# Performance work log

Hardware: AMD Instinct MI355X
Metric: run time of the kernel (lower is better)

The kernel has to match this reference:

```python
import jax, jax.numpy as jnp
import numpy as np

DT = 0.01
SIGMA_RECUR = 0.005
SIGMA_INPUT = 0.05


def setup_inputs() -> dict:
    key = jax.random.key(0)
    ks = jax.random.split(key, 13)
    B, T, I, H = 64, 1000, 4, 512
    H2 = 2 * H
    return {
        "inp": jax.random.normal(ks[0], (B, T, I), jnp.float32),
        "hn": jax.random.uniform(ks[1], (1, B, H2), jnp.float32),
        "x": jax.random.normal(ks[2], (1, B, H2), jnp.float32),
        "inhib_stim": jax.random.normal(ks[3], (B, H2), jnp.float32),
        "perturb_hid": jax.random.normal(ks[4], (T,), jnp.float32),
        "perturb_inp": jax.random.normal(ks[5], (T,), jnp.float32),
        "str2str": jax.random.uniform(ks[6], (H, H), jnp.float32, -0.01, 0.01),
        "alm2alm": jax.random.uniform(ks[7], (H, H), jnp.float32, -0.01, 0.01),
        "alm2str": jax.random.uniform(ks[8], (H, H), jnp.float32, -0.01, 0.01),
        "str2alm": jax.random.uniform(ks[9], (H, H), jnp.float32, -0.01, 0.01),
        "inp_weight": jax.random.uniform(ks[10], (I, H2), jnp.float32, -0.01, 0.01),
        "fc1_w": jax.random.uniform(ks[11], (1, H2), jnp.float32, -0.03, 0.03),
        "fc1_b": jnp.zeros((1,), jnp.float32),
    }


def reference(inp, hn, x, inhib_stim, perturb_hid, perturb_inp,
              str2str, alm2alm, alm2str, str2alm, inp_weight, fc1_w, fc1_b):
    H = str2str.shape[0]
    # W_rec: [[str2str, alm2str], [str2alm, alm2alm]] -> (2H, 2H)
    W_rec = jnp.concatenate([
        jnp.concatenate([str2str, alm2str], axis=1),
        jnp.concatenate([str2alm, alm2alm], axis=1),
    ], axis=0)
    str_mask = jnp.concatenate([jnp.ones((H,), inp.dtype), jnp.zeros((H,), inp.dtype)])
    alm_mask = jnp.concatenate([jnp.zeros((H,), inp.dtype), jnp.ones((H,), inp.dtype)])

    # scalar per-step noise, as in the original (single Normal draw per t)
    ph = jnp.sqrt(2 * DT * SIGMA_RECUR ** 2) * perturb_hid  # [T]
    pi = jnp.sqrt(2 * DT * SIGMA_INPUT ** 2) * perturb_inp  # [T]

    h0 = hn[0]  # [B, 2H]
    x0 = x[0]   # [B, 2H]

    def step(carry, xs_t):
        h_prev, x_prev = carry
        inp_t, ph_t, pi_t = xs_t  # inp_t: [B, I]
        drive = (inp_t + pi_t) @ inp_weight  # [B, 2H]
        x_new = x_prev + DT * (-x_prev + h_prev @ W_rec.T
                               + drive * str_mask + inhib_stim) + ph_t
        h_new = jax.nn.relu(x_new)
        return (h_new, x_new), (h_new, x_new)

    inp_t_major = jnp.transpose(inp, (1, 0, 2))  # [T, B, I]
    (_, _), (hs, xs) = jax.lax.scan(step, (h0, x0), (inp_t_major, ph, pi))

    rnn_out = jnp.transpose(hs, (1, 0, 2))  # [B, T, 2H]
    x_out = jnp.transpose(xs, (1, 0, 2))    # [B, T, 2H]
    hn_last = rnn_out[:, -1, :][None]       # [1, B, 2H]
    x_last = x_out[:, -1, :][None]
    out = (rnn_out * alm_mask) @ fc1_w.T + fc1_b  # [B, T, 1]
    return (out, hn_last, rnn_out, x_last, x_out)
```

## Files before the change

kernel.cpp:

```cpp
#include <hip/hip_runtime.h>
#include <hip/hip_bf16.h>

#define TT 1000
#define HH 512
#define HH2 1024
#define DT_ 0.01f
#define PH_SCALE 7.0710678118654745e-4f
#define PI_SCALE 7.0710678118654745e-3f

typedef short s16x8 __attribute__((ext_vector_type(8)));
typedef float f32x4 __attribute__((ext_vector_type(4)));
typedef unsigned u32x4 __attribute__((ext_vector_type(4)));

#define SIGN32  0x80008000u
#define STRIP32 0x7fff7fffu

static __device__ __forceinline__ unsigned short bf16_bits(float f) {
    union { __hip_bfloat16 h; unsigned short u; } b; b.h = __float2bfloat16(f); return b.u;
}
static __device__ __forceinline__ unsigned pat32(int t) {
    const unsigned tg = ((unsigned)t >> 1) & 3u;
    return ((tg & 1u) << 15) | ((tg & 2u) << 30);
}

__global__ __launch_bounds__(256, 1) void rnn_persistent(
    const float* __restrict__ inp, const float* __restrict__ hn,
    const float* __restrict__ x0g, const float* __restrict__ inhib,
    const float* __restrict__ ph, const float* __restrict__ pig,
    const float* __restrict__ s2s, const float* __restrict__ a2a,
    const float* __restrict__ a2s, const float* __restrict__ s2a,
    const float* __restrict__ iw,
    float* __restrict__ rnn_out, float* __restrict__ x_out,
    unsigned* __restrict__ hbuf)
{
    const int tid  = threadIdx.x;
    const int wid  = tid >> 6;
    const int lane = tid & 63;
    const int b    = blockIdx.x;
    const int g    = b >> 4;
    const int qb   = b & 15;
    const int l15  = lane & 15;
    const int lq   = lane >> 4;
    const int r8   = l15 & 7;
    const int g8   = g * 8;
    const int icol = (qb * 4 + wid) * 16 + l15;
    const bool owner = (lq < 2);
    const int rowbase = g8 + (lq & 1) * 4;

    __shared__ __align__(16) unsigned short hlds[2][8 * 1024];

    {
        float h0v[4];
        #pragma unroll
        for (int r = 0; r < 4; ++r)
            h0v[r] = hn[(size_t)(rowbase + r) * HH2 + icol];
        float prr[4];
        #pragma unroll
        for (int r = 0; r < 4; ++r) prr[r] = __shfl_xor(h0v[r], 1);
        if (owner && !(l15 & 1)) {
            const unsigned p0 = pat32(0);
            #pragma unroll
            for (int r = 0; r < 4; ++r) {
                const unsigned val = (((unsigned)bf16_bits(h0v[r]) |
                                       ((unsigned)bf16_bits(prr[r]) << 16)) & STRIP32);
                __hip_atomic_store(hbuf + (size_t)(g8 + lq * 4 + r) * 512 + (icol >> 1),
                                   val | p0, __ATOMIC_RELAXED, __HIP_MEMORY_SCOPE_AGENT);
            }
        }
    }

    s16x8 wfr[32];
    #pragma unroll
    for (int kc = 0; kc < 32; ++kc) {
        const int j = kc * 32 + lq * 8;
        const float* src;
        if (icol < HH) src = (j < HH) ? (s2s + (size_t)icol * HH + j)
                                      : (a2s + (size_t)icol * HH + (j - HH));
        else           src = (j < HH) ? (s2a + (size_t)(icol - HH) * HH + j)
                                      : (a2a + (size_t)(icol - HH) * HH + (j - HH));
        const float4 f0 = *(const float4*)(src);
        const float4 f1 = *(const float4*)(src + 4);
        union { s16x8 vv; unsigned short us[8]; } u;
        u.us[0] = bf16_bits(f0.x); u.us[1] = bf16_bits(f0.y);
        u.us[2] = bf16_bits(f0.z); u.us[3] = bf16_bits(f0.w);
        u.us[4] = bf16_bits(f1.x); u.us[5] = bf16_bits(f1.y);
        u.us[6] = bf16_bits(f1.z); u.us[7] = bf16_bits(f1.w);
        wfr[kc] = u.vv;
    }

    const bool isStr = (icol < HH);
    float iw0 = 0.f, iw1 = 0.f, iw2 = 0.f, iw3 = 0.f;
    if (isStr) {
        iw0 = iw[icol]; iw1 = iw[HH2 + icol];
        iw2 = iw[2 * HH2 + icol]; iw3 = iw[3 * HH2 + icol];
    }
    float xr[4], inh[4];
    float4 ipf[4];
    #pragma unroll
    for (int r = 0; r < 4; ++r) {
        const int bi = rowbase + r;
        xr[r]  = x0g[(size_t)bi * HH2 + icol];
        inh[r] = inhib[(size_t)bi * HH2 + icol];
        ipf[r] = *(const float4*)(inp + ((size_t)bi * TT + 0) * 4);
    }
    float phv = ph[0], piv = pig[0];

    auto stage = [&](int t) {
        const unsigned* srcs = hbuf + (size_t)(t & 1) * 32768 + (size_t)g8 * 512;
        char* dst = (char*)hlds[t & 1];
        const unsigned p32 = pat32(t);
        u32x4 c[4];
        #pragma unroll
        for (int rd = 0; rd < 4; ++rd) {
            const int gch = tid + rd * 256;
            const int row = gch >> 7, c16 = gch & 127;
            const unsigned* p = srcs + row * 512 + c16 * 4;
            asm volatile("global_load_dwordx4 %0, %1, off sc0 sc1"
                         : "=v"(c[rd]) : "v"(p) : "memory");
        }
        asm volatile("s_waitcnt vmcnt(0)" ::: "memory");
        unsigned fm = 0u;
        #pragma unroll
        for (int rd = 0; rd < 4; ++rd) {
            const unsigned y = ((c[rd][0] ^ p32) | (c[rd][1] ^ p32) |
                                (c[rd][2] ^ p32) | (c[rd][3] ^ p32)) & SIGN32;
            if (y) fm |= 1u << rd;
        }
        float burn = (float)tid;
        while (fm) {
            #pragma unroll
            for (int rd = 0; rd < 4; ++rd) {
                if (fm & (1u << rd)) {
                    const int gch = tid + rd * 256;
                    const int row = gch >> 7, c16 = gch & 127;
                    const unsigned* p = srcs + row * 512 + c16 * 4;
                    asm volatile("global_load_dwordx4 %0, %1, off sc0 sc1"
                                 : "=v"(c[rd]) : "v"(p) : "memory");
                }
            }
            #pragma unroll
            for (int z = 0; z < 8; ++z) burn = fmaf(burn, 1.000001f, 0.5f);
            asm volatile("" :: "v"(burn));
            asm volatile("s_waitcnt vmcnt(0)" ::: "memory");
            #pragma unroll
            for (int rd = 0; rd < 4; ++rd) {
                if (fm & (1u << rd)) {
                    const unsigned y = ((c[rd][0] ^ p32) | (c[rd][1] ^ p32) |
                                        (c[rd][2] ^ p32) | (c[rd][3] ^ p32)) & SIGN32;
                    if (!y) fm &= ~(1u << rd);
                }
            }
        }
        #pragma unroll
        for (int rd = 0; rd < 4; ++rd) {
            const int gch = tid + rd * 256;
            const int row = gch >> 7, c16 = gch & 127;
            u32x4 s;
            s[0] = c[rd][0] & STRIP32; s[1] = c[rd][1] & STRIP32;
            s[2] = c[rd][2] & STRIP32; s[3] = c[rd][3] & STRIP32;
            *(u32x4*)(dst + row * 2048 + ((c16 ^ row) * 16)) = s;
        }
    };

    stage(0);
    __syncthreads();

    #pragma unroll 1
    for (int t = 0; t < TT; ++t) {
        f32x4 acc[4] = {{0,0,0,0},{0,0,0,0},{0,0,0,0},{0,0,0,0}};
        const char* arow = (const char*)hlds[t & 1] + r8 * 2048;
        #pragma unroll
        for (int kc = 0; kc < 32; ++kc) {
            s16x8 a0 = *(const s16x8*)(arow + (((kc << 2 | lq) ^ r8) * 16));
            acc[kc & 3] = __builtin_amdgcn_mfma_f32_16x16x32_bf16(a0, wfr[kc], acc[kc & 3], 0, 0, 0);
        }

        const float phs = PH_SCALE * phv;
        const float pis = PI_SCALE * piv;
        float xn_[4], hv_[4];
        #pragma unroll
        for (int r = 0; r < 4; ++r) {
            const float rec = acc[0][r] + acc[1][r] + acc[2][r] + acc[3][r];
            float drive = 0.f;
            if (isStr) drive = (ipf[r].x + pis) * iw0 + (ipf[r].y + pis) * iw1 +
                               (ipf[r].z + pis) * iw2 + (ipf[r].w + pis) * iw3;
            const float xp = xr[r];
            const float xn = xp + DT_ * (-xp + rec + drive + inh[r]) + phs;
            const float hv = fmaxf(xn, 0.f);
            xr[r] = xn; xn_[r] = xn; hv_[r] = hv;
        }

        if (t + 1 < TT) {
            unsigned* nxt = hbuf + (size_t)((t + 1) & 1) * 32768;
            const unsigned pn = pat32(t + 1);
            float prr[4];
            #pragma unroll
            for (int r = 0; r < 4; ++r) prr[r] = __shfl_xor(hv_[r], 1);
            if (owner && !(l15 & 1)) {
                #pragma unroll
                for (int r = 0; r < 4; ++r) {
                    const unsigned val = (((unsigned)bf16_bits(hv_[r]) |
                                           ((unsigned)bf16_bits(prr[r]) << 16)) & STRIP32);
                    __hip_atomic_store(nxt + (size_t)(g8 + lq * 4 + r) * 512 + (icol >> 1),
                                       val | pn, __ATOMIC_RELAXED, __HIP_MEMORY_SCOPE_AGENT);
                }
            }
        }

        if (owner) {
            #pragma unroll
            for (int r = 0; r < 4; ++r) {
                const int bi = g8 + lq * 4 + r;
                const size_t o = ((size_t)bi * TT + t) * HH2 + icol;
                rnn_out[o] = hv_[r];
                x_out[o]   = xn_[r];
            }
        }

        const int tn = (t + 1 < TT) ? (t + 1) : t;
        #pragma unroll
        for (int r = 0; r < 4; ++r)
            ipf[r] = *(const float4*)(inp + ((size_t)(rowbase + r) * TT + tn) * 4);
        phv = ph[tn]; piv = pig[tn];

        if (t + 1 < TT) stage(t + 1);
        __syncthreads();
    }
}

__global__ __launch_bounds__(256) void fc1_kernel(
    const float* __restrict__ rnn_out, const float* __restrict__ fc1_w,
    const float* __restrict__ fc1_b, float* __restrict__ out)
{
    const int wid = blockIdx.x * 4 + (threadIdx.x >> 6);
    const int lane = threadIdx.x & 63;
    const float* p = rnn_out + (size_t)wid * HH2 + HH + lane * 8;
    const float* w = fc1_w + HH + lane * 8;
    f32x4 v0 = *(const f32x4*)(p);
    f32x4 v1 = *(const f32x4*)(p + 4);
    f32x4 w0 = *(const f32x4*)(w);
    f32x4 w1 = *(const f32x4*)(w + 4);
    float s = v0[0]*w0[0] + v0[1]*w0[1] + v0[2]*w0[2] + v0[3]*w0[3]
            + v1[0]*w1[0] + v1[1]*w1[1] + v1[2]*w1[2] + v1[3]*w1[3];
    #pragma unroll
    for (int off = 32; off; off >>= 1) s += __shfl_xor(s, off);
    if (lane == 0) out[wid] = s + fc1_b[0];
}

__global__ __launch_bounds__(256) void last_kernel(
    const float* __restrict__ rnn_out, const float* __restrict__ x_out,
    float* __restrict__ hn_last, float* __restrict__ x_last)
{
    const int idx = blockIdx.x * 256 + threadIdx.x;
    const int b = idx >> 10;
    const int i = idx & 1023;
    const size_t o = ((size_t)b * TT + (TT - 1)) * HH2 + i;
    hn_last[idx] = rnn_out[o];
    x_last[idx]  = x_out[o];
}

extern "C" void kernel_launch(void* const* d_in, const int* in_sizes, int n_in,
                              void* d_out, int out_size, void* d_ws, size_t ws_size,
                              hipStream_t stream) {
    const float* inp   = (const float*)d_in[0];
    const float* hn    = (const float*)d_in[1];
    const float* x     = (const float*)d_in[2];
    const float* inhib = (const float*)d_in[3];
    const float* ph    = (const float*)d_in[4];
    const float* pi    = (const float*)d_in[5];
    const float* s2s   = (const float*)d_in[6];
    const float* a2a   = (const float*)d_in[7];
    const float* a2s   = (const float*)d_in[8];
    const float* s2a   = (const float*)d_in[9];
    const float* iw    = (const float*)d_in[10];
    const float* fw    = (const float*)d_in[11];
    const float* fb    = (const float*)d_in[12];

    float* out     = (float*)d_out;
    float* hn_last = out + 64000;
    float* rnn_out = out + 129536;
    float* x_last  = out + 65665536;
    float* x_out   = out + 65731072;

    unsigned* hbuf = (unsigned*)d_ws;

    rnn_persistent<<<128, 256, 0, stream>>>(inp, hn, x, inhib, ph, pi,
                                            s2s, a2a, a2s, s2a, iw,
                                            rnn_out, x_out, hbuf);
    fc1_kernel<<<16000, 256, 0, stream>>>(rnn_out, fw, fb, out);
    last_kernel<<<256, 256, 0, stream>>>(rnn_out, x_out, hn_last, x_last);
}
```

Baseline: 2.404 ms.

## Split batch into 4-row groups across 256 persistent blocks

The persistent RNN kernel now gives each block 4 batch rows instead of 8, doubling the grid to 256 blocks. Each block stages half as much hidden state per step, and the stage loop writes each chunk to LDS as soon as its flag matches rather than after all chunks arrive. The aim is to cut per-step staging latency and spread the output stores over more CUs. In exchange, half of each MFMA's 16 rows now hold duplicated rows, and twice as many blocks take part in the cross-block flag synchronisation.

New measurement: 2.119 ms. 1.13x faster.

```diff
diff --git a/kernel.cpp b/kernel.cpp
--- a/kernel.cpp
+++ b/kernel.cpp
@@ -41,19 +41,18 @@
     const int qb   = b & 15;
     const int l15  = lane & 15;
     const int lq   = lane >> 4;
-    const int r8   = l15 & 7;
-    const int g8   = g * 8;
+    const int r4   = l15 & 3;
+    const int g4   = g * 4;
     const int icol = (qb * 4 + wid) * 16 + l15;
-    const bool owner = (lq < 2);
-    const int rowbase = g8 + (lq & 1) * 4;
-
-    __shared__ __align__(16) unsigned short hlds[2][8 * 1024];
+    const bool owner = (lq == 0);
+
+    __shared__ __align__(16) unsigned short hlds[2][4 * 1024];
 
     {
         float h0v[4];
         #pragma unroll
         for (int r = 0; r < 4; ++r)
-            h0v[r] = hn[(size_t)(rowbase + r) * HH2 + icol];
+            h0v[r] = hn[(size_t)(g4 + r) * HH2 + icol];
         float prr[4];
         #pragma unroll
         for (int r = 0; r < 4; ++r) prr[r] = __shfl_xor(h0v[r], 1);
@@ -63,7 +62,7 @@
             for (int r = 0; r < 4; ++r) {
                 const unsigned val = (((unsigned)bf16_bits(h0v[r]) |
                                        ((unsigned)bf16_bits(prr[r]) << 16)) & STRIP32);
-                __hip_atomic_store(hbuf + (size_t)(g8 + lq * 4 + r) * 512 + (icol >> 1),
+                __hip_atomic_store(hbuf + (size_t)(g4 + r) * 512 + (icol >> 1),
                                    val | p0, __ATOMIC_RELAXED, __HIP_MEMORY_SCOPE_AGENT);
             }
         }
@@ -98,7 +97,7 @@
     float4 ipf[4];
     #pragma unroll
     for (int r = 0; r < 4; ++r) {
-        const int bi = rowbase + r;
+        const int bi = g4 + r;
         xr[r]  = x0g[(size_t)bi * HH2 + icol];
         inh[r] = inhib[(size_t)bi * HH2 + icol];
         ipf[r] = *(const float4*)(inp + ((size_t)bi * TT + 0) * 4);
@@ -106,59 +105,41 @@
     float phv = ph[0], piv = pig[0];
 
     auto stage = [&](int t) {
-        const unsigned* srcs = hbuf + (size_t)(t & 1) * 32768 + (size_t)g8 * 512;
+        const unsigned* srcs = hbuf + (size_t)(t & 1) * 32768 + (size_t)g4 * 512;
         char* dst = (char*)hlds[t & 1];
         const unsigned p32 = pat32(t);
-        u32x4 c[4];
-        #pragma unroll
-        for (int rd = 0; rd < 4; ++rd) {
-            const int gch = tid + rd * 256;
-            const int row = gch >> 7, c16 = gch & 127;
-            const unsigned* p = srcs + row * 512 + c16 * 4;
-            asm volatile("global_load_dwordx4 %0, %1, off sc0 sc1"
-                         : "=v"(c[rd]) : "v"(p) : "memory");
-        }
+        const int row0 = tid >> 7,         c160 = tid & 127;
+        const int row1 = (tid + 256) >> 7, c161 = tid & 127;
+        const unsigned* p0 = srcs + row0 * 512 + c160 * 4;
+        const unsigned* p1 = srcs + row1 * 512 + c161 * 4;
+        char* d0 = dst + row0 * 2048 + ((c160 ^ row0) * 16);
+        char* d1 = dst + row1 * 2048 + ((c161 ^ row1) * 16);
+        u32x4 c0, c1;
+        asm volatile("global_load_dwordx4 %0, %1, off sc0 sc1" : "=v"(c0) : "v"(p0) : "memory");
+        asm volatile("global_load_dwordx4 %0, %1, off sc0 sc1" : "=v"(c1) : "v"(p1) : "memory");
         asm volatile("s_waitcnt vmcnt(0)" ::: "memory");
-        unsigned fm = 0u;
-        #pragma unroll
-        for (int rd = 0; rd < 4; ++rd) {
-            const unsigned y = ((c[rd][0] ^ p32) | (c[rd][1] ^ p32) |
-                                (c[rd][2] ^ p32) | (c[rd][3] ^ p32)) & SIGN32;
-            if (y) fm |= 1u << rd;
-        }
+        bool f0 = (((c0[0] ^ p32) | (c0[1] ^ p32) | (c0[2] ^ p32) | (c0[3] ^ p32)) & SIGN32) != 0u;
+        bool f1 = (((c1[0] ^ p32) | (c1[1] ^ p32) | (c1[2] ^ p32) | (c1[3] ^ p32)) & SIGN32) != 0u;
+        if (!f0) { u32x4 s = {c0[0] & STRIP32, c0[1] & STRIP32, c0[2] & STRIP32, c0[3] & STRIP32};
+                   *(u32x4*)d0 = s; }
+        if (!f1) { u32x4 s = {c1[0] & STRIP32, c1[1] & STRIP32, c1[2] & STRIP32, c1[3] & STRIP32};
+                   *(u32x4*)d1 = s; }
         float burn = (float)tid;
-        while (fm) {
-            #pragma unroll
-            for (int rd = 0; rd < 4; ++rd) {
-                if (fm & (1u << rd)) {
-                    const int gch = tid + rd * 256;
-                    const int row = gch >> 7, c16 = gch & 127;
-                    const unsigned* p = srcs + row * 512 + c16 * 4;
-                    asm volatile("global_load_dwordx4 %0, %1, off sc0 sc1"
-                                 : "=v"(c[rd]) : "v"(p) : "memory");
-                }
-            }
+        while (f0 || f1) {
+            if (f0) asm volatile("global_load_dwordx4 %0, %1, off sc0 sc1" : "=v"(c0) : "v"(p0) : "memory");
+            if (f1) asm volatile("global_load_dwordx4 %0, %1, off sc0 sc1" : "=v"(c1) : "v"(p1) : "memory");
             #pragma unroll
             for (int z = 0; z < 8; ++z) burn = fmaf(burn, 1.000001f, 0.5f);
             asm volatile("" :: "v"(burn));
             asm volatile("s_waitcnt vmcnt(0)" ::: "memory");
-            #pragma unroll
-            for (int rd = 0; rd < 4; ++rd) {
-                if (fm & (1u << rd)) {
-                    const unsigned y = ((c[rd][0] ^ p32) | (c[rd][1] ^ p32) |
-                                        (c[rd][2] ^ p32) | (c[rd][3] ^ p32)) & SIGN32;
-                    if (!y) fm &= ~(1u << rd);
-                }
-            }
-        }
-        #pragma unroll
-        for (int rd = 0; rd < 4; ++rd) {
-            const int gch = tid + rd * 256;
-            const int row = gch >> 7, c16 = gch & 127;
-            u32x4 s;
-            s[0] = c[rd][0] & STRIP32; s[1] = c[rd][1] & STRIP32;
-            s[2] = c[rd][2] & STRIP32; s[3] = c[rd][3] & STRIP32;
-            *(u32x4*)(dst + row * 2048 + ((c16 ^ row) * 16)) = s;
+            if (f0 && ((((c0[0] ^ p32) | (c0[1] ^ p32) | (c0[2] ^ p32) | (c0[3] ^ p32)) & SIGN32) == 0u)) {
+                u32x4 s = {c0[0] & STRIP32, c0[1] & STRIP32, c0[2] & STRIP32, c0[3] & STRIP32};
+                *(u32x4*)d0 = s; f0 = false;
+            }
+            if (f1 && ((((c1[0] ^ p32) | (c1[1] ^ p32) | (c1[2] ^ p32) | (c1[3] ^ p32)) & SIGN32) == 0u)) {
+                u32x4 s = {c1[0] & STRIP32, c1[1] & STRIP32, c1[2] & STRIP32, c1[3] & STRIP32};
+                *(u32x4*)d1 = s; f1 = false;
+            }
         }
     };
 
@@ -168,10 +149,10 @@
     #pragma unroll 1
     for (int t = 0; t < TT; ++t) {
         f32x4 acc[4] = {{0,0,0,0},{0,0,0,0},{0,0,0,0},{0,0,0,0}};
-        const char* arow = (const char*)hlds[t & 1] + r8 * 2048;
+        const char* arow = (const char*)hlds[t & 1] + r4 * 2048;
         #pragma unroll
         for (int kc = 0; kc < 32; ++kc) {
-            s16x8 a0 = *(const s16x8*)(arow + (((kc << 2 | lq) ^ r8) * 16));
+            s16x8 a0 = *(const s16x8*)(arow + (((kc << 2 | lq) ^ r4) * 16));
             acc[kc & 3] = __builtin_amdgcn_mfma_f32_16x16x32_bf16(a0, wfr[kc], acc[kc & 3], 0, 0, 0);
         }
 
@@ -201,7 +182,7 @@
                 for (int r = 0; r < 4; ++r) {
                     const unsigned val = (((unsigned)bf16_bits(hv_[r]) |
                                            ((unsigned)bf16_bits(prr[r]) << 16)) & STRIP32);
-                    __hip_atomic_store(nxt + (size_t)(g8 + lq * 4 + r) * 512 + (icol >> 1),
+                    __hip_atomic_store(nxt + (size_t)(g4 + r) * 512 + (icol >> 1),
                                        val | pn, __ATOMIC_RELAXED, __HIP_MEMORY_SCOPE_AGENT);
                 }
             }
@@ -210,7 +191,7 @@
         if (owner) {
             #pragma unroll
             for (int r = 0; r < 4; ++r) {
-                const int bi = g8 + lq * 4 + r;
+                const int bi = g4 + r;
                 const size_t o = ((size_t)bi * TT + t) * HH2 + icol;
                 rnn_out[o] = hv_[r];
                 x_out[o]   = xn_[r];
@@ -220,7 +201,7 @@
         const int tn = (t + 1 < TT) ? (t + 1) : t;
         #pragma unroll
         for (int r = 0; r < 4; ++r)
-            ipf[r] = *(const float4*)(inp + ((size_t)(rowbase + r) * TT + tn) * 4);
+            ipf[r] = *(const float4*)(inp + ((size_t)(g4 + r) * TT + tn) * 4);
         phv = ph[tn]; piv = pig[tn];
 
         if (t + 1 < TT) stage(t + 1);
@@ -284,7 +265,7 @@
 
     unsigned* hbuf = (unsigned*)d_ws;
 
-    rnn_persistent<<<128, 256, 0, stream>>>(inp, hn, x, inhib, ph, pi,
+    rnn_persistent<<<256, 256, 0, stream>>>(inp, hn, x, inhib, ph, pi,
                                             s2s, a2a, a2s, s2a, iw,
                                             rnn_out, x_out, hbuf);
     fc1_kernel<<<16000, 256, 0, stream>>>(rnn_out, fw, fb, out);
```
